# Performance work log

Measured on AMD Instinct MI355X. Metric: run time of the kernel, lower is better.

The kernel has to match this reference:

```python
import jax, jax.numpy as jnp
import numpy as np

HEADS = 8
LN_EPS = 1e-5
BN_EPS = 1e-5
MIN_EPS, MAX_EPS = 1e-4, 10.0


def _ln(x, g, b):
    m = x.mean(-1, keepdims=True)
    v = x.var(-1, keepdims=True)
    return (x - m) / jnp.sqrt(v + LN_EPS) * g + b


def _pos2d(a, b, dim, temperature=10000.0):
    # faithful to build_2d_sincos_position_embedding(w=a, h=b)
    grid_a = jnp.arange(a, dtype=jnp.float32)
    grid_b = jnp.arange(b, dtype=jnp.float32)
    ga, gb = jnp.meshgrid(grid_a, grid_b, indexing='ij')  # (a, b)
    pos_dim = dim // 4
    omega = 1.0 / (temperature ** (jnp.arange(pos_dim, dtype=jnp.float32) / pos_dim))
    out_a = ga.flatten()[:, None] * omega[None]
    out_b = gb.flatten()[:, None] * omega[None]
    return jnp.concatenate([jnp.sin(out_a), jnp.cos(out_a), jnp.sin(out_b), jnp.cos(out_b)], axis=1)  # (a*b, dim)


def _avgpool(x, k):
    bb, cc, H, W = x.shape
    return x.reshape(bb, cc, H // k, k, W // k, k).mean((3, 5))


def setup_inputs() -> dict:
    key = jax.random.key(0)
    c1, c2, bs = 256, 512, 16
    ks = jax.random.split(key, 12)

    def lin(k, o, i):
        return (jax.random.normal(k, (o, i), jnp.float32) * (1.0 / np.sqrt(i))).astype(jnp.float32)

    return {
        'a3': jax.random.normal(ks[0], (bs, c1, 80, 80), jnp.float32),
        'a4': jax.random.normal(ks[1], (bs, c2, 40, 40), jnp.float32),
        'conv_w': lin(ks[2], c1, c2), 'conv_b': jnp.zeros((c1,), jnp.float32),
        'bn_g': jnp.ones((c1,), jnp.float32), 'bn_b': jnp.zeros((c1,), jnp.float32),
        'q_w': lin(ks[3], c1, c1), 'q_b': jnp.zeros((c1,), jnp.float32),
        'q_ln_g': jnp.ones((c1,), jnp.float32), 'q_ln_b': jnp.zeros((c1,), jnp.float32),
        'k_w': lin(ks[4], c1, c1), 'k_b': jnp.zeros((c1,), jnp.float32),
        'k_ln_g': jnp.ones((c1,), jnp.float32), 'k_ln_b': jnp.zeros((c1,), jnp.float32),
        'v_w': lin(ks[5], c1, c1), 'v_b': jnp.zeros((c1,), jnp.float32),
        'out_w': lin(ks[6], c1, c1), 'out_b': jnp.zeros((c1,), jnp.float32),
        'lin1_w': lin(ks[7], 4 * c1, c1), 'lin1_b': jnp.zeros((4 * c1,), jnp.float32),
        'lin2_w': lin(ks[8], c1, 4 * c1), 'lin2_b': jnp.zeros((c1,), jnp.float32),
        'norm1_g': jnp.ones((c1,), jnp.float32), 'norm1_b': jnp.zeros((c1,), jnp.float32),
        'norm2_g': jnp.ones((c1,), jnp.float32), 'norm2_b': jnp.zeros((c1,), jnp.float32),
        'idx': 10,
    }


def reference(a3, a4, conv_w, conv_b, bn_g, bn_b, q_w, q_b, q_ln_g, q_ln_b,
              k_w, k_b, k_ln_g, k_ln_b, v_w, v_b, out_w, out_b,
              lin1_w, lin1_b, lin2_w, lin2_b, norm1_g, norm1_b, norm2_g, norm2_b, idx):
    a3 = jnp.nan_to_num(a3, nan=0.0, posinf=1e4, neginf=-1e4)
    a4 = jnp.nan_to_num(a4, nan=0.0, posinf=1e4, neginf=-1e4)
    orig_a3, orig_a4 = a3, a4

    # high_to_low_embed: 1x1 conv + BatchNorm (eval: running_mean=0, running_var=1)
    a4e = jnp.einsum('bchw,oc->bohw', a4, conv_w) + conv_b[None, :, None, None]
    a4e = a4e / jnp.sqrt(1.0 + BN_EPS) * bn_g[None, :, None, None] + bn_b[None, :, None, None]

    if idx == 10:
        a3d = _avgpool(a3, 2)
    else:
        a3d = _avgpool(a3, 4)
        a4e = _avgpool(a4e, 2)

    bs, c, h, w = a3d.shape
    tgt = h * w
    src = a4e.shape[2] * a4e.shape[3]

    residual = a3d.reshape(bs, c, tgt).transpose(0, 2, 1)      # (bs, tgt, c)
    a3f = a3d.reshape(bs, c, tgt).transpose(2, 0, 1)            # (tgt, bs, c)
    a4f = a4e.reshape(bs, c, src).transpose(2, 0, 1)            # (src, bs, c)

    pos = _pos2d(h, w, c)[:, None, :]                           # (h*w, 1, c)
    a3f = a3f + pos
    a4f = a4f + pos                                             # src == tgt by construction

    Q = jax.nn.relu(_ln(a3f @ q_w.T + q_b, q_ln_g, q_ln_b))
    K = jax.nn.relu(_ln(a4f @ k_w.T + k_b, k_ln_g, k_ln_b))
    V = a4f @ v_w.T + v_b

    hd = c // HEADS
    Q = Q.reshape(tgt, bs, HEADS, hd).transpose(1, 2, 0, 3)     # (b, h, tgt, hd)
    K = K.reshape(src, bs, HEADS, hd).transpose(1, 2, 0, 3)
    V = V.reshape(src, bs, HEADS, hd).transpose(1, 2, 0, 3)

    m = max(src, tgt)
    wi = (np.pi / 2) * jnp.arange(1, m + 1, dtype=jnp.float32) / m  # (m,)
    sq = jnp.sin(wi[:tgt])[None, None, :, None]
    cq = jnp.cos(wi[:tgt])[None, None, :, None]
    sk = jnp.sin(wi[:src])[None, None, :, None]
    ck = jnp.cos(wi[:src])[None, None, :, None]
    Q_ = jnp.concatenate([Q * sq, Q * cq], -1)                  # (b, h, tgt, 2hd)
    K_ = jnp.concatenate([K * sk, K * ck], -1)                  # (b, h, src, 2hd)

    KV = jnp.einsum('bhsd,bhse->bhde', K_, V)                   # (b, h, 2hd, hd)
    Zden = jnp.einsum('bhld,bhd->bhl', Q_, K_.sum(2))
    Z = 1.0 / jnp.clip(Zden, MIN_EPS, MAX_EPS)
    attn = jnp.einsum('bhld,bhde->bhle', Q_, KV) * Z[..., None]  # (b, h, tgt, hd)

    attn = attn.transpose(2, 0, 1, 3).reshape(tgt, bs, c)
    out = (attn @ out_w.T + out_b).transpose(1, 0, 2)           # (bs, tgt, c)
    out = _ln(out, norm1_g, norm1_b)
    out = residual + out

    res2 = out
    ff = jax.nn.gelu(out @ lin1_w.T + lin1_b, approximate=False) @ lin2_w.T + lin2_b
    ff = _ln(ff, norm2_g, norm2_b)
    out = res2 + ff

    a3_sa = out.transpose(0, 2, 1).reshape(bs, c, h, w)
    a3_sa = jax.image.resize(a3_sa, orig_a3.shape, 'bilinear')  # align_corners=False
    a3_sa = a3_sa * orig_a3

    B4, C4, H4, W4 = orig_a4.shape
    a4_up = jax.image.resize(orig_a4, (B4, C4, 2 * H4, 2 * W4), 'bilinear')
    return (a3_sa, a4_up)
```

## Files before the change

### kernel.cpp

```cpp
#include <hip/hip_runtime.h>
#include <math.h>


typedef __attribute__((ext_vector_type(8))) short bf16x8;
typedef __attribute__((ext_vector_type(8))) unsigned short us8;
typedef __attribute__((ext_vector_type(4))) unsigned short us4h;
typedef __attribute__((ext_vector_type(4))) float f32x4;

__device__ __forceinline__ unsigned short f2bf(float f) {
  unsigned int u = __float_as_uint(f);
  u += 0x7fff + ((u >> 16) & 1);
  return (unsigned short)(u >> 16);
}
__device__ __forceinline__ float bf2f(unsigned short u) {
  return __uint_as_float(((unsigned int)u) << 16);
}

__global__ __launch_bounds__(256) void wprep_kernel(
    const float* __restrict__ cw, const float* __restrict__ qw,
    const float* __restrict__ kw, const float* __restrict__ vw,
    const float* __restrict__ ow, const float* __restrict__ l1w,
    const float* __restrict__ l2w, unsigned short* __restrict__ wbf) {
  int gid = blockIdx.x * 256 + threadIdx.x;
  size_t e0 = (size_t)gid * 8;
  const float* src; size_t off;
  if (e0 < 131072)      { src = cw;  off = e0; }
  else if (e0 < 196608) { src = qw;  off = e0 - 131072; }
  else if (e0 < 262144) { src = kw;  off = e0 - 196608; }
  else if (e0 < 327680) { src = vw;  off = e0 - 262144; }
  else if (e0 < 393216) { src = ow;  off = e0 - 327680; }
  else if (e0 < 655360) { src = l1w; off = e0 - 393216; }
  else                  { src = l2w; off = e0 - 655360; }
  float4 v0 = *(const float4*)(src + off);
  float4 v1 = *(const float4*)(src + off + 4);
  us8 r;
  r[0] = f2bf(v0.x); r[1] = f2bf(v0.y); r[2] = f2bf(v0.z); r[3] = f2bf(v0.w);
  r[4] = f2bf(v1.x); r[5] = f2bf(v1.y); r[6] = f2bf(v1.z); r[7] = f2bf(v1.w);
  *(us8*)(wbf + e0) = r;
}

__global__ void pos_kernel(float* __restrict__ pos) {
  int s = blockIdx.x, c = threadIdx.x;
  int y = s / 40, x = s - y * 40;
  int quad = c >> 6, i = c & 63;
  float omega = expf(-(float)i * (9.2103403719761836f / 64.0f));
  float coord = (quad < 2) ? (float)y : (float)x;
  float a = coord * omega;
  pos[s * 256 + c] = (quad & 1) ? cosf(a) : sinf(a);
}

__global__ __launch_bounds__(640) void avgpool_kernel(
    const float* __restrict__ a3, const float* __restrict__ pos,
    unsigned short* __restrict__ X3) {
  __shared__ float buf2[256][44];
  int y = blockIdx.x, b = blockIdx.y;
  int tid = threadIdx.x;
  int x2 = tid % 20, cq = tid / 20;
#pragma unroll
  for (int it = 0; it < 8; ++it) {
    int c = cq + 32 * it;
    const float* p = a3 + (((size_t)(b * 256 + c) * 80 + 2 * y) * 80 + x2 * 4);
    float4 r0 = *(const float4*)p;
    float4 r1 = *(const float4*)(p + 80);
    buf2[c][2 * x2]     = 0.25f * ((r0.x + r0.y) + (r1.x + r1.y));
    buf2[c][2 * x2 + 1] = 0.25f * ((r0.z + r0.w) + (r1.z + r1.w));
  }
  __syncthreads();
  size_t t0 = (size_t)b * 1600 + y * 40;
  int sbase = y * 40;
#pragma unroll
  for (int it = 0; it < 4; ++it) {
    int idx = it * 640 + tid;
    int c = idx & 255, xq = idx >> 8;
    int x0 = xq * 4;
    float4 v = *(const float4*)&buf2[c][x0];
#pragma unroll
    for (int j = 0; j < 4; ++j) {
      float pv = pos[(size_t)(sbase + x0 + j) * 256 + c];
      float vv = (j == 0) ? v.x : (j == 1) ? v.y : (j == 2) ? v.z : v.w;
      X3[(t0 + x0 + j) * 256 + c] = f2bf(vv + pv);
    }
  }
}

__global__ __launch_bounds__(256) void a4t_kernel(
    const float* __restrict__ a4, unsigned short* __restrict__ a4t) {
  __shared__ float buf[64][65];
  int s0 = blockIdx.x * 64, k0 = blockIdx.y * 64, b = blockIdx.z;
  const float* src = a4 + ((size_t)b * 512 + k0) * 1600 + s0;
#pragma unroll
  for (int p = 0; p < 4; ++p) {
    int idx = p * 256 + threadIdx.x;
    int kk = idx >> 4, s4 = (idx & 15) * 4;
    float4 v = *(const float4*)(src + (size_t)kk * 1600 + s4);
    buf[kk][s4 + 0] = v.x; buf[kk][s4 + 1] = v.y;
    buf[kk][s4 + 2] = v.z; buf[kk][s4 + 3] = v.w;
  }
  __syncthreads();
  unsigned short* dst = a4t + ((size_t)b * 1600 + s0) * 512 + k0;
#pragma unroll
  for (int p = 0; p < 4; ++p) {
    int idx = p * 256 + threadIdx.x;
    int ss = idx >> 4, kq = (idx & 15) * 4;
    us4h v;
    v[0] = f2bf(buf[kq + 0][ss]); v[1] = f2bf(buf[kq + 1][ss]);
    v[2] = f2bf(buf[kq + 2][ss]); v[3] = f2bf(buf[kq + 3][ss]);
    *(us4h*)(dst + (size_t)ss * 512 + kq) = v;
  }
}

template<int EPI>
__global__ __launch_bounds__(256) void fgemm(
    const unsigned short* __restrict__ A, const unsigned short* __restrict__ W,
    const float* __restrict__ bias, void* __restrict__ outp,
    const int K, const int ldN,
    const float* __restrict__ posb,
    const float* __restrict__ g1, const float* __restrict__ b1,
    const unsigned short* __restrict__ res) {
  __shared__ __align__(16) unsigned short Albs[64][40];
  __shared__ __align__(16) unsigned short Wlds[256][40];
  __shared__ float part[2][64][2];
  int tid = threadIdx.x;
  int lane = tid & 63, w = tid >> 6;
  int m0 = (w >> 1) * 32, n0 = (w & 1) * 128;
  int g = lane >> 4, cl = lane & 15;
  int t0 = blockIdx.x * 64, o0 = blockIdx.y * 256;
  f32x4 acc[2][8] = {};
  int arr = tid >> 2, acol = (tid & 3) * 8;

  for (int k0 = 0; k0 < K; k0 += 32) {
    __syncthreads();
    *(us8*)&Albs[arr][acol] = *(const us8*)(A + (size_t)(t0 + arr) * K + (k0 + acol));
#pragma unroll
    for (int p = 0; p < 4; ++p) {
      int idx = p * 256 + tid;
      int rr = idx >> 2, cc = (idx & 3) * 8;
      *(us8*)&Wlds[rr][cc] = *(const us8*)(W + (size_t)(o0 + rr) * K + (k0 + cc));
    }
    __syncthreads();
    bf16x8 af[2], bw[8];
#pragma unroll
    for (int ms = 0; ms < 2; ++ms)
      af[ms] = *(const bf16x8*)&Albs[m0 + ms * 16 + cl][g * 8];
#pragma unroll
    for (int ns = 0; ns < 8; ++ns)
      bw[ns] = *(const bf16x8*)&Wlds[n0 + ns * 16 + cl][g * 8];
#pragma unroll
    for (int ms = 0; ms < 2; ++ms)
#pragma unroll
      for (int ns = 0; ns < 8; ++ns)
        acc[ms][ns] = __builtin_amdgcn_mfma_f32_16x16x32_bf16(af[ms], bw[ns], acc[ms][ns], 0, 0, 0);
  }

  float bv[8];
#pragma unroll
  for (int ns = 0; ns < 8; ++ns) bv[ns] = bias[o0 + n0 + ns * 16 + cl];
  int sbase = t0 % 1600;

  if constexpr (EPI == 2 || EPI == 3 || EPI == 5) {
#pragma unroll
    for (int ms = 0; ms < 2; ++ms) {
#pragma unroll
      for (int i = 0; i < 4; ++i) {
        float p = 0.f, q = 0.f;
#pragma unroll
        for (int ns = 0; ns < 8; ++ns) {
          float v = acc[ms][ns][i] + bv[ns];
          p += v; q += v * v;
        }
        p += __shfl_xor(p, 1); q += __shfl_xor(q, 1);
        p += __shfl_xor(p, 2); q += __shfl_xor(q, 2);
        p += __shfl_xor(p, 4); q += __shfl_xor(q, 4);
        p += __shfl_xor(p, 8); q += __shfl_xor(q, 8);
        if (cl == 0) {
          int rl = m0 + ms * 16 + g * 4 + i;
          part[w & 1][rl][0] = p;
          part[w & 1][rl][1] = q;
        }
      }
    }
    __syncthreads();
  }

  if constexpr (EPI == 5) {
    float* of = (float*)outp;
    int bb = t0 / 1600;
#pragma unroll
    for (int ms = 0; ms < 2; ++ms) {
      int rl0 = m0 + ms * 16 + g * 4;
      float mean[4], inv[4];
#pragma unroll
      for (int i = 0; i < 4; ++i) {
        float sp = part[0][rl0 + i][0] + part[1][rl0 + i][0];
        float sq = part[0][rl0 + i][1] + part[1][rl0 + i][1];
        mean[i] = sp * (1.f / 256.f);
        float var = sq * (1.f / 256.f) - mean[i] * mean[i];
        inv[i] = rsqrtf(var + 1e-5f);
      }
#pragma unroll
      for (int ns = 0; ns < 8; ++ns) {
        int col = n0 + ns * 16 + cl;
        float gg = g1[col], b2 = b1[col];
        float4 y;
#pragma unroll
        for (int i = 0; i < 4; ++i) {
          float v = acc[ms][ns][i] + bv[ns];
          float yy = (v - mean[i]) * inv[i] * gg + b2;
          yy += bf2f(res[(size_t)(t0 + rl0 + i) * 256 + col]);
          if (i == 0) y.x = yy; else if (i == 1) y.y = yy;
          else if (i == 2) y.z = yy; else y.w = yy;
        }
        *(float4*)(of + ((size_t)(bb * 256 + col) * 1600) + sbase + rl0) = y;
      }
    }
    return;
  }

  unsigned short* ob = (unsigned short*)outp;
#pragma unroll
  for (int ms = 0; ms < 2; ++ms) {
#pragma unroll
    for (int i = 0; i < 4; ++i) {
      int rl = m0 + ms * 16 + g * 4 + i;
      int t = t0 + rl;
      float mean = 0.f, inv = 0.f;
      if constexpr (EPI == 2 || EPI == 3) {
        float sp = part[0][rl][0] + part[1][rl][0];
        float sq = part[0][rl][1] + part[1][rl][1];
        mean = sp * (1.f / 256.f);
        float var = sq * (1.f / 256.f) - mean * mean;
        inv = rsqrtf(var + 1e-5f);
      }
#pragma unroll
      for (int ns = 0; ns < 8; ++ns) {
        int col = n0 + ns * 16 + cl;
        float v = acc[ms][ns][i] + bv[ns];
        size_t oidx = (size_t)t * ldN + o0 + col;
        if constexpr (EPI == 0) {
          ob[oidx] = f2bf(v);
        } else if constexpr (EPI == 1) {
          const float is = 0.99999500003749968f;
          float y = v * (is * g1[col]) + b1[col] + posb[(size_t)(sbase + rl) * 256 + col];
          ob[oidx] = f2bf(y);
        } else if constexpr (EPI == 2) {
          float y = (v - mean) * inv * g1[col] + b1[col];
          ob[oidx] = f2bf(fmaxf(y, 0.f));
        } else if constexpr (EPI == 3) {
          float y = (v - mean) * inv * g1[col] + b1[col];
          y += bf2f(res[(size_t)t * 256 + col]) - posb[(size_t)(sbase + rl) * 256 + col];
          ob[oidx] = f2bf(y);
        } else if constexpr (EPI == 4) {
          float y = 0.5f * v * (1.f + erff(v * 0.7071067811865475f));
          ob[oidx] = f2bf(y);
        }
      }
    }
  }
}

__global__ __launch_bounds__(256) void kv_kernel(
    const unsigned short* __restrict__ Kb, const unsigned short* __restrict__ Vb,
    float* __restrict__ KVp, float* __restrict__ Ksp) {
  __shared__ float Kc[64][32];
  __shared__ float Vc[64][32];
  __shared__ float sv[64], cv[64];
  __shared__ float red[4][64];
  int bx = blockIdx.x;
  int bh = bx / 5, sp = bx - bh * 5;
  int b = bh >> 3, h = bh & 7;
  int tid = threadIdx.x;
  int e = tid & 31, dg = tid >> 5;
  int d4 = dg * 4;
  int dks = tid & 63, partid = tid >> 6;
  float accs[4] = {0.f, 0.f, 0.f, 0.f};
  float accc[4] = {0.f, 0.f, 0.f, 0.f};
  float ks = 0.f;
  size_t base = ((size_t)b * 1600) * 256 + h * 32;
  for (int s0 = sp * 320; s0 < sp * 320 + 320; s0 += 64) {
    __syncthreads();
#pragma unroll
    for (int p = 0; p < 8; ++p) {
      int si = dg + p * 8;
      Kc[si][e] = bf2f(Kb[base + (size_t)(s0 + si) * 256 + e]);
      Vc[si][e] = bf2f(Vb[base + (size_t)(s0 + si) * 256 + e]);
    }
    if (tid < 64) {
      float wv = 1.5707963267948966f * (float)(s0 + tid + 1) * (1.0f / 1600.0f);
      sv[tid] = sinf(wv);
      cv[tid] = cosf(wv);
    }
    __syncthreads();
#pragma unroll 8
    for (int si = 0; si < 64; ++si) {
      float vv = Vc[si][e];
      float sn = sv[si], cs = cv[si];
      float4 k4 = *(const float4*)&Kc[si][d4];
      float p0 = k4.x * vv, p1 = k4.y * vv, p2 = k4.z * vv, p3 = k4.w * vv;
      accs[0] = fmaf(p0, sn, accs[0]); accc[0] = fmaf(p0, cs, accc[0]);
      accs[1] = fmaf(p1, sn, accs[1]); accc[1] = fmaf(p1, cs, accc[1]);
      accs[2] = fmaf(p2, sn, accs[2]); accc[2] = fmaf(p2, cs, accc[2]);
      accs[3] = fmaf(p3, sn, accs[3]); accc[3] = fmaf(p3, cs, accc[3]);
    }
#pragma unroll 4
    for (int q = 0; q < 16; ++q) {
      int si = partid * 16 + q;
      float kvv = (dks < 32) ? Kc[si][dks] * sv[si] : Kc[si][dks - 32] * cv[si];
      ks += kvv;
    }
  }
  red[partid][dks] = ks;
  __syncthreads();
  size_t ob = (size_t)sp * 128 + bh;
  if (tid < 64)
    Ksp[ob * 64 + tid] = (red[0][tid] + red[1][tid]) + (red[2][tid] + red[3][tid]);
#pragma unroll
  for (int i = 0; i < 4; ++i) {
    KVp[ob * 2048 + (d4 + i) * 32 + e] = accs[i];
    KVp[ob * 2048 + (32 + d4 + i) * 32 + e] = accc[i];
  }
}

__global__ __launch_bounds__(256) void kvred_kernel(
    const float* __restrict__ KVp, const float* __restrict__ Ksp,
    float* __restrict__ KV, float* __restrict__ Ks) {
  int bh = blockIdx.x, tid = threadIdx.x;
  size_t o = (size_t)bh * 2048 + tid * 8;
  float4 s0 = make_float4(0, 0, 0, 0), s1 = make_float4(0, 0, 0, 0);
#pragma unroll
  for (int sp = 0; sp < 5; ++sp) {
    const float* p = KVp + ((size_t)sp * 128 + bh) * 2048 + tid * 8;
    float4 a = *(const float4*)p;
    float4 b2 = *(const float4*)(p + 4);
    s0.x += a.x; s0.y += a.y; s0.z += a.z; s0.w += a.w;
    s1.x += b2.x; s1.y += b2.y; s1.z += b2.z; s1.w += b2.w;
  }
  *(float4*)(KV + o) = s0;
  *(float4*)(KV + o + 4) = s1;
  if (tid < 64) {
    float t = 0.f;
#pragma unroll
    for (int sp = 0; sp < 5; ++sp) t += Ksp[((size_t)sp * 128 + bh) * 64 + tid];
    Ks[bh * 64 + tid] = t;
  }
}

__global__ __launch_bounds__(256) void attn_kernel(
    const unsigned short* __restrict__ Qb, const float* __restrict__ KV,
    const float* __restrict__ Ksum, unsigned short* __restrict__ attn) {
  int grp = threadIdx.x >> 5;
  int e = threadIdx.x & 31;
  int t = blockIdx.x * 8 + grp;
  int b = t / 1600, s = t - b * 1600;
  float wv = 1.5707963267948966f * (float)(s + 1) * (1.0f / 1600.0f);
  float sq = sinf(wv), cq = cosf(wv);
  const unsigned short* qrow = Qb + (size_t)t * 256;
  for (int h = 0; h < 8; ++h) {
    int bh = b * 8 + h;
    const float* kv = KV + (size_t)bh * 2048;
    const float* ksm = Ksum + (size_t)bh * 64;
    float qe = bf2f(qrow[h * 32 + e]);
    float zp = qe * (sq * ksm[e] + cq * ksm[32 + e]);
    zp += __shfl_xor(zp, 1); zp += __shfl_xor(zp, 2);
    zp += __shfl_xor(zp, 4); zp += __shfl_xor(zp, 8); zp += __shfl_xor(zp, 16);
    float acc = 0.f;
#pragma unroll 8
    for (int d = 0; d < 32; ++d) {
      float qv = bf2f(qrow[h * 32 + d]);
      acc = fmaf(qv * sq, kv[d * 32 + e], acc);
      acc = fmaf(qv * cq, kv[(32 + d) * 32 + e], acc);
    }
    float zc = fminf(fmaxf(zp, 1e-4f), 10.0f);
    attn[(size_t)t * 256 + h * 32 + e] = f2bf(acc * (1.0f / zc));
  }
}

__device__ __forceinline__ float4 up_row4(const float* sm, int Y, int q) {
  float fy = Y * 0.5f - 0.25f;
  int iy = (int)floorf(fy);
  float dy = fy - (float)iy;
  int y0 = iy < 0 ? 0 : iy;
  int y1 = (iy + 1) > 39 ? 39 : (iy + 1);
  const float* r0 = sm + y0 * 40;
  const float* r1 = sm + y1 * 40;
  int cm1 = (2 * q - 1) < 0 ? 0 : (2 * q - 1);
  int cp2 = (2 * q + 2) > 39 ? 39 : (2 * q + 2);
  float w1 = 1.f - dy;
  float s0 = w1 * r0[cm1]       + dy * r1[cm1];
  float s1 = w1 * r0[2 * q]     + dy * r1[2 * q];
  float s2 = w1 * r0[2 * q + 1] + dy * r1[2 * q + 1];
  float s3 = w1 * r0[cp2]       + dy * r1[cp2];
  float4 o;
  o.x = 0.25f * s0 + 0.75f * s1;
  o.y = 0.75f * s1 + 0.25f * s2;
  o.z = 0.25f * s1 + 0.75f * s2;
  o.w = 0.75f * s2 + 0.25f * s3;
  return o;
}

__global__ __launch_bounds__(256) void upsample_mul_kernel(
    const float* __restrict__ src, const float* __restrict__ a3, float* __restrict__ out) {
  __shared__ float sm[1600];
  int c = blockIdx.x, b = blockIdx.y;
  size_t sbase = ((size_t)b * 256 + c) * 1600;
  for (int i = threadIdx.x; i < 400; i += 256)
    *(float4*)&sm[i * 4] = *(const float4*)(src + sbase + i * 4);
  __syncthreads();
  size_t obase = ((size_t)b * 256 + c) * 6400;
  for (int i = threadIdx.x; i < 1600; i += 256) {
    int Y = i / 20, q = i - Y * 20;
    float4 o = up_row4(sm, Y, q);
    float4 m = *(const float4*)(a3 + obase + i * 4);
    o.x *= m.x; o.y *= m.y; o.z *= m.z; o.w *= m.w;
    *(float4*)(out + obase + i * 4) = o;
  }
}

__global__ __launch_bounds__(256) void upsample_kernel(
    const float* __restrict__ src, float* __restrict__ out) {
  __shared__ float sm[1600];
  int c = blockIdx.x, b = blockIdx.y;
  size_t sbase = ((size_t)b * 512 + c) * 1600;
  for (int i = threadIdx.x; i < 400; i += 256)
    *(float4*)&sm[i * 4] = *(const float4*)(src + sbase + i * 4);
  __syncthreads();
  size_t obase = ((size_t)b * 512 + c) * 6400;
  for (int i = threadIdx.x; i < 1600; i += 256) {
    int Y = i / 20, q = i - Y * 20;
    float4 o = up_row4(sm, Y, q);
    *(float4*)(out + obase + i * 4) = o;
  }
}

extern "C" void kernel_launch(void* const* d_in, const int* in_sizes, int n_in,
                              void* d_out, int out_size, void* d_ws, size_t ws_size,
                              hipStream_t stream) {
  const float* a3     = (const float*)d_in[0];
  const float* a4     = (const float*)d_in[1];
  const float* conv_w = (const float*)d_in[2];
  const float* conv_b = (const float*)d_in[3];
  const float* bn_g   = (const float*)d_in[4];
  const float* bn_b   = (const float*)d_in[5];
  const float* q_w    = (const float*)d_in[6];
  const float* q_b    = (const float*)d_in[7];
  const float* q_ln_g = (const float*)d_in[8];
  const float* q_ln_b = (const float*)d_in[9];
  const float* k_w    = (const float*)d_in[10];
  const float* k_b    = (const float*)d_in[11];
  const float* k_ln_g = (const float*)d_in[12];
  const float* k_ln_b = (const float*)d_in[13];
  const float* v_w    = (const float*)d_in[14];
  const float* v_b    = (const float*)d_in[15];
  const float* out_w  = (const float*)d_in[16];
  const float* out_b  = (const float*)d_in[17];
  const float* lin1_w = (const float*)d_in[18];
  const float* lin1_b = (const float*)d_in[19];
  const float* lin2_w = (const float*)d_in[20];
  const float* lin2_b = (const float*)d_in[21];
  const float* n1_g   = (const float*)d_in[22];
  const float* n1_b   = (const float*)d_in[23];
  const float* n2_g   = (const float*)d_in[24];
  const float* n2_b   = (const float*)d_in[25];
  (void)in_sizes; (void)n_in; (void)out_size; (void)ws_size;

  float* ws = (float*)d_ws;
  float* pos  = ws + 0;
  unsigned short* wbf = (unsigned short*)(ws + 409600);
  float* KV   = ws + 868352;
  float* Ks   = ws + 1130496;
  float* KVp  = ws + 1138688;
  float* Ksp  = ws + 2449408;
  unsigned short* X3b  = (unsigned short*)(ws + 2490368);
  unsigned short* X4b  = (unsigned short*)(ws + 5767168);
  unsigned short* Qbb  = (unsigned short*)(ws + 9043968);
  unsigned short* Kbb  = (unsigned short*)(ws + 12320768);
  unsigned short* Vbb  = (unsigned short*)(ws + 15597568);
  unsigned short* o1b  = (unsigned short*)(ws + 18874368);
  unsigned short* a4tb = (unsigned short*)(ws + 22151168);
  unsigned short* ffhb = (unsigned short*)(ws + 22151168);
  float* a3p  = ws + 9043968;

  const unsigned short* w_conv = wbf;
  const unsigned short* w_q    = wbf + 131072;
  const unsigned short* w_k    = wbf + 196608;
  const unsigned short* w_v    = wbf + 262144;
  const unsigned short* w_o    = wbf + 327680;
  const unsigned short* w_l1   = wbf + 393216;
  const unsigned short* w_l2   = wbf + 655360;

  float* out0 = (float*)d_out;
  float* out1f = out0 + (size_t)16 * 256 * 80 * 80;

  wprep_kernel<<<448, 256, 0, stream>>>(conv_w, q_w, k_w, v_w, out_w, lin1_w, lin2_w, wbf);
  pos_kernel<<<1600, 256, 0, stream>>>(pos);
  avgpool_kernel<<<dim3(40, 16), 640, 0, stream>>>(a3, pos, X3b);
  a4t_kernel<<<dim3(25, 8, 16), 256, 0, stream>>>(a4, a4tb);
  fgemm<1><<<dim3(400, 1), 256, 0, stream>>>(a4tb, w_conv, conv_b, X4b, 512, 256, pos, bn_g, bn_b, nullptr);
  fgemm<2><<<dim3(400, 1), 256, 0, stream>>>(X3b, w_q, q_b, Qbb, 256, 256, nullptr, q_ln_g, q_ln_b, nullptr);
  fgemm<2><<<dim3(400, 1), 256, 0, stream>>>(X4b, w_k, k_b, Kbb, 256, 256, nullptr, k_ln_g, k_ln_b, nullptr);
  fgemm<0><<<dim3(400, 1), 256, 0, stream>>>(X4b, w_v, v_b, Vbb, 256, 256, nullptr, nullptr, nullptr, nullptr);
  kv_kernel<<<640, 256, 0, stream>>>(Kbb, Vbb, KVp, Ksp);
  kvred_kernel<<<128, 256, 0, stream>>>(KVp, Ksp, KV, Ks);
  attn_kernel<<<3200, 256, 0, stream>>>(Qbb, KV, Ks, Kbb );
  fgemm<3><<<dim3(400, 1), 256, 0, stream>>>(Kbb, w_o, out_b, o1b, 256, 256, pos, n1_g, n1_b, X3b);
  fgemm<4><<<dim3(400, 4), 256, 0, stream>>>(o1b, w_l1, lin1_b, ffhb, 256, 1024, nullptr, nullptr, nullptr, nullptr);
  fgemm<5><<<dim3(400, 1), 256, 0, stream>>>(ffhb, w_l2, lin2_b, a3p, 1024, 256, nullptr, n2_g, n2_b, o1b);
  upsample_mul_kernel<<<dim3(256, 16), 256, 0, stream>>>(a3p, a3, out0);
  upsample_kernel<<<dim3(512, 16), 256, 0, stream>>>(a4, out1f);
}
```

Baseline: 453.9 us.

## Load GEMM tiles via direct global-to-LDS loads and remap warps to column strips

The fused GEMM now stages A and W tiles with global_load_lds 16-byte direct loads instead of register round-trips, dropping the LDS row padding so each wave writes contiguous 16-row blocks. Each wave now owns all 64 rows and a 64-column strip rather than a 32x128 quadrant, and the LayerNorm partial sums grow to four per-wave slots. The goal is to cut VGPR traffic and instruction count in the load phase. The unpadded LDS rows may cause bank conflicts on fragment reads, and there is no waitcnt beyond the barrier, so correctness depends on the compiler inserting vmcnt waits.

```diff
diff --git a/kernel.cpp b/kernel.cpp
--- a/kernel.cpp
+++ b/kernel.cpp
@@ -14,6 +14,12 @@
 }
 __device__ __forceinline__ float bf2f(unsigned short u) {
   return __uint_as_float(((unsigned int)u) << 16);
+}
+
+__device__ __forceinline__ void gload16(const void* g, void* l) {
+  __builtin_amdgcn_global_load_lds(
+      (const __attribute__((address_space(1))) void*)g,
+      (__attribute__((address_space(3))) void*)l, 16, 0, 0);
 }
 
 __global__ __launch_bounds__(256) void wprep_kernel(
@@ -117,54 +123,63 @@
     const float* __restrict__ posb,
     const float* __restrict__ g1, const float* __restrict__ b1,
     const unsigned short* __restrict__ res) {
-  __shared__ __align__(16) unsigned short Albs[64][40];
-  __shared__ __align__(16) unsigned short Wlds[256][40];
-  __shared__ float part[2][64][2];
+  __shared__ __align__(16) unsigned short Albs[64][32];
+  __shared__ __align__(16) unsigned short Wlds[256][32];
+  __shared__ float part[4][64][2];
   int tid = threadIdx.x;
   int lane = tid & 63, w = tid >> 6;
-  int m0 = (w >> 1) * 32, n0 = (w & 1) * 128;
   int g = lane >> 4, cl = lane & 15;
+  int n0 = w * 64;
   int t0 = blockIdx.x * 64, o0 = blockIdx.y * 256;
-  f32x4 acc[2][8] = {};
-  int arr = tid >> 2, acol = (tid & 3) * 8;
+  f32x4 acc[4][4] = {};
+
+  int arow = lane >> 2, acol = (lane & 3) * 8;
+  const unsigned short* ag  = A + (size_t)(t0 + w * 16 + arow) * K + acol;
+  const unsigned short* wg0 = W + (size_t)(o0 + (w)      * 16 + arow) * K + acol;
+  const unsigned short* wg1 = W + (size_t)(o0 + (4 + w)  * 16 + arow) * K + acol;
+  const unsigned short* wg2 = W + (size_t)(o0 + (8 + w)  * 16 + arow) * K + acol;
+  const unsigned short* wg3 = W + (size_t)(o0 + (12 + w) * 16 + arow) * K + acol;
+  unsigned short* al  = &Albs[w * 16][0];
+  unsigned short* wl0 = &Wlds[(w) * 16][0];
+  unsigned short* wl1 = &Wlds[(4 + w) * 16][0];
+  unsigned short* wl2 = &Wlds[(8 + w) * 16][0];
+  unsigned short* wl3 = &Wlds[(12 + w) * 16][0];
 
   for (int k0 = 0; k0 < K; k0 += 32) {
     __syncthreads();
-    *(us8*)&Albs[arr][acol] = *(const us8*)(A + (size_t)(t0 + arr) * K + (k0 + acol));
-#pragma unroll
-    for (int p = 0; p < 4; ++p) {
-      int idx = p * 256 + tid;
-      int rr = idx >> 2, cc = (idx & 3) * 8;
-      *(us8*)&Wlds[rr][cc] = *(const us8*)(W + (size_t)(o0 + rr) * K + (k0 + cc));
-    }
+    gload16(ag + k0, al);
+    gload16(wg0 + k0, wl0);
+    gload16(wg1 + k0, wl1);
+    gload16(wg2 + k0, wl2);
+    gload16(wg3 + k0, wl3);
     __syncthreads();
-    bf16x8 af[2], bw[8];
-#pragma unroll
-    for (int ms = 0; ms < 2; ++ms)
-      af[ms] = *(const bf16x8*)&Albs[m0 + ms * 16 + cl][g * 8];
-#pragma unroll
-    for (int ns = 0; ns < 8; ++ns)
+    bf16x8 af[4], bw[4];
+#pragma unroll
+    for (int ms = 0; ms < 4; ++ms)
+      af[ms] = *(const bf16x8*)&Albs[ms * 16 + cl][g * 8];
+#pragma unroll
+    for (int ns = 0; ns < 4; ++ns)
       bw[ns] = *(const bf16x8*)&Wlds[n0 + ns * 16 + cl][g * 8];
 #pragma unroll
-    for (int ms = 0; ms < 2; ++ms)
-#pragma unroll
-      for (int ns = 0; ns < 8; ++ns)
+    for (int ms = 0; ms < 4; ++ms)
+#pragma unroll
+      for (int ns = 0; ns < 4; ++ns)
         acc[ms][ns] = __builtin_amdgcn_mfma_f32_16x16x32_bf16(af[ms], bw[ns], acc[ms][ns], 0, 0, 0);
   }
 
-  float bv[8];
-#pragma unroll
-  for (int ns = 0; ns < 8; ++ns) bv[ns] = bias[o0 + n0 + ns * 16 + cl];
+  float bv[4];
+#pragma unroll
+  for (int ns = 0; ns < 4; ++ns) bv[ns] = bias[o0 + n0 + ns * 16 + cl];
   int sbase = t0 % 1600;
 
   if constexpr (EPI == 2 || EPI == 3 || EPI == 5) {
 #pragma unroll
-    for (int ms = 0; ms < 2; ++ms) {
+    for (int ms = 0; ms < 4; ++ms) {
 #pragma unroll
       for (int i = 0; i < 4; ++i) {
         float p = 0.f, q = 0.f;
 #pragma unroll
-        for (int ns = 0; ns < 8; ++ns) {
+        for (int ns = 0; ns < 4; ++ns) {
           float v = acc[ms][ns][i] + bv[ns];
           p += v; q += v * v;
         }
@@ -173,9 +188,9 @@
         p += __shfl_xor(p, 4); q += __shfl_xor(q, 4);
         p += __shfl_xor(p, 8); q += __shfl_xor(q, 8);
         if (cl == 0) {
-          int rl = m0 + ms * 16 + g * 4 + i;
-          part[w & 1][rl][0] = p;
-          part[w & 1][rl][1] = q;
+          int rl = ms * 16 + g * 4 + i;
+          part[w][rl][0] = p;
+          part[w][rl][1] = q;
         }
       }
     }
@@ -186,19 +201,21 @@
     float* of = (float*)outp;
     int bb = t0 / 1600;
 #pragma unroll
-    for (int ms = 0; ms < 2; ++ms) {
-      int rl0 = m0 + ms * 16 + g * 4;
+    for (int ms = 0; ms < 4; ++ms) {
+      int rl0 = ms * 16 + g * 4;
       float mean[4], inv[4];
 #pragma unroll
       for (int i = 0; i < 4; ++i) {
-        float sp = part[0][rl0 + i][0] + part[1][rl0 + i][0];
-        float sq = part[0][rl0 + i][1] + part[1][rl0 + i][1];
+        float sp = (part[0][rl0 + i][0] + part[1][rl0 + i][0]) +
+                   (part[2][rl0 + i][0] + part[3][rl0 + i][0]);
+        float sq = (part[0][rl0 + i][1] + part[1][rl0 + i][1]) +
+                   (part[2][rl0 + i][1] + part[3][rl0 + i][1]);
         mean[i] = sp * (1.f / 256.f);
         float var = sq * (1.f / 256.f) - mean[i] * mean[i];
         inv[i] = rsqrtf(var + 1e-5f);
       }
 #pragma unroll
-      for (int ns = 0; ns < 8; ++ns) {
+      for (int ns = 0; ns < 4; ++ns) {
         int col = n0 + ns * 16 + cl;
         float gg = g1[col], b2 = b1[col];
         float4 y;
@@ -218,21 +235,21 @@
 
   unsigned short* ob = (unsigned short*)outp;
 #pragma unroll
-  for (int ms = 0; ms < 2; ++ms) {
+  for (int ms = 0; ms < 4; ++ms) {
 #pragma unroll
     for (int i = 0; i < 4; ++i) {
-      int rl = m0 + ms * 16 + g * 4 + i;
+      int rl = ms * 16 + g * 4 + i;
       int t = t0 + rl;
       float mean = 0.f, inv = 0.f;
       if constexpr (EPI == 2 || EPI == 3) {
-        float sp = part[0][rl][0] + part[1][rl][0];
-        float sq = part[0][rl][1] + part[1][rl][1];
+        float sp = (part[0][rl][0] + part[1][rl][0]) + (part[2][rl][0] + part[3][rl][0]);
+        float sq = (part[0][rl][1] + part[1][rl][1]) + (part[2][rl][1] + part[3][rl][1]);
         mean = sp * (1.f / 256.f);
         float var = sq * (1.f / 256.f) - mean * mean;
         inv = rsqrtf(var + 1e-5f);
       }
 #pragma unroll
-      for (int ns = 0; ns < 8; ++ns) {
+      for (int ns = 0; ns < 4; ++ns) {
         int col = n0 + ns * 16 + cl;
         float v = acc[ms][ns][i] + bv[ns];
         size_t oidx = (size_t)t * ldN + o0 + col;
```

Result: faster. 434.9 us (-4.2%).
